# Kernel tuning notes

Hardware: AMD Instinct MI355X
Metric: run time of the kernel (lower is better)

## Reference

```python
import jax, jax.numpy as jnp
import numpy as np

T, B, E, H = 2048, 2, 2048, 16
HD = E // H
SCALE = HD ** -0.5
NEG = -1e9  # large-negative additive mask (finite, safe in fp32/bf16)


def setup_inputs() -> dict:
    key = jax.random.key(0)
    ks = jax.random.split(key, 6)
    query = jax.random.normal(ks[0], (T, B, E), dtype=jnp.float32)
    # causal additive mask, as metaseq builds for decoder self-attention
    attn_mask = jnp.where(jnp.tril(jnp.ones((T, T), dtype=bool)), 0.0, NEG).astype(jnp.float32)
    # combined qkv projection: rows ordered [K | V | Q] per split_tensor_along_last_dim
    qkv_w = jax.random.normal(ks[1], (3 * E, E), dtype=jnp.float32) * (1.0 / np.sqrt(2 * E))
    qkv_b = jax.random.uniform(ks[2], (3 * E,), dtype=jnp.float32, minval=-1, maxval=1) / np.sqrt(E)
    out_w = jax.random.normal(ks[3], (E, E), dtype=jnp.float32) * (1.0 / np.sqrt(2 * E))
    out_b = jax.random.uniform(ks[4], (E,), dtype=jnp.float32, minval=-1, maxval=1) / np.sqrt(E)
    return {"query": query, "attn_mask": attn_mask, "qkv_w": qkv_w,
            "qkv_b": qkv_b, "out_w": out_w, "out_b": out_b}


def reference(query, attn_mask, qkv_w, qkv_b, out_w, out_b):
    t, b, e = query.shape
    # fused QKV projection (ColumnParallelLinear, world_size=1)
    kvq = jnp.einsum('tbe,fe->tbf', query, qkv_w) + qkv_b  # [T,B,3E]
    k, v, q = kvq[..., :e], kvq[..., e:2 * e], kvq[..., 2 * e:]
    q = q * SCALE
    q = q.reshape(t, b, H, HD)
    k = k.reshape(t, b, H, HD)
    v = v.reshape(t, b, H, HD)
    # explicit QK^T bmm -> [B,H,T,S]
    scores = jnp.einsum('tbhd,sbhd->bhts', q, k) + attn_mask[None, None]
    probs = jax.nn.softmax(scores, axis=-1)  # dropout p=0 -> identity
    ctx = jnp.einsum('bhts,sbhd->tbhd', probs, v).reshape(t, b, e)
    # RowParallelLinear out_proj (skip_bias_add in the original; bias added here)
    out = jnp.einsum('tbe,fe->tbf', ctx, out_w) + out_b
    return out
```

## Files before the change

kernel.cpp:

```cpp
#include <hip/hip_runtime.h>
#include <hip/hip_bf16.h>
#include <stdint.h>

#define T_DIM 2048
#define B_DIM 2
#define E_DIM 2048
#define H_DIM 16
#define HD_DIM 128
#define F_DIM 6144
#define ROWS 4096
#define KVB 64

#define QK_SCALE 0.08838834764831845f
#define LOG2E    1.4426950408889634f
#define RESCALE_THR 8.0f

typedef __bf16 bf16_t;
typedef __bf16 bf16x8 __attribute__((ext_vector_type(8)));
typedef __bf16 bf16x4 __attribute__((ext_vector_type(4)));
typedef float  f32x4  __attribute__((ext_vector_type(4)));

__device__ __forceinline__ void gll16(const void* g, void* l) {
  __builtin_amdgcn_global_load_lds((const __attribute__((address_space(1))) void*)g,
                                   (__attribute__((address_space(3))) void*)l, 16, 0, 0);
}

__global__ void cvt_f32_bf16(const float* __restrict__ src, bf16_t* __restrict__ dst, int n4) {
  int i = blockIdx.x * blockDim.x + threadIdx.x;
  int stride = gridDim.x * blockDim.x;
  for (; i < n4; i += stride) {
    float4 v = ((const float4*)src)[i];
    bf16x4 o;
    o[0] = (bf16_t)v.x; o[1] = (bf16_t)v.y; o[2] = (bf16_t)v.z; o[3] = (bf16_t)v.w;
    ((bf16x4*)dst)[i] = o;
  }
}

template<int EPI>
__launch_bounds__(256, 2)
__global__ void gemm_bt(const bf16_t* __restrict__ A, const bf16_t* __restrict__ Bm,
                        const float* __restrict__ bias, void* __restrict__ Cout,
                        int N, int K, int nbn, float qscale, int qcol0)
{
  __shared__ __align__(16) bf16_t As[128][64];
  __shared__ __align__(16) bf16_t Bs[128][64];

  int bid = blockIdx.x;
  int nwg = gridDim.x;
  int cpx = nwg >> 3;
  int swz = (bid & 7) * cpx + (bid >> 3);
  int bm = swz / nbn, bn = swz % nbn;

  int tid = threadIdx.x;
  int lane = tid & 63, wid = tid >> 6;
  int lr = lane & 15, lg = lane >> 4;
  int wm = wid >> 1, wn = wid & 1;

  f32x4 acc[4][4] = {};

  int srow8 = tid >> 3;
  int schunk = tid & 7;

  const bf16_t* gA = A + (size_t)(bm * 128) * K;
  const bf16_t* gB = Bm + (size_t)(bn * 128) * K;

  for (int k0 = 0; k0 < K; k0 += 64) {
    #pragma unroll
    for (int i = 0; i < 4; ++i) {
      int row = i * 32 + srow8;
      int sc = schunk ^ (row & 7);
      gll16(gA + (size_t)row * K + k0 + sc * 8, &As[row][schunk * 8]);
    }
    #pragma unroll
    for (int i = 0; i < 4; ++i) {
      int row = i * 32 + srow8;
      int sc = schunk ^ (row & 7);
      gll16(gB + (size_t)row * K + k0 + sc * 8, &Bs[row][schunk * 8]);
    }
    __syncthreads();

    #pragma unroll
    for (int kk = 0; kk < 2; ++kk) {
      bf16x8 af[4], bfr[4];
      #pragma unroll
      for (int mi = 0; mi < 4; ++mi) {
        int row = wm * 64 + mi * 16 + lr;
        int ch = (kk * 4 + lg) ^ (row & 7);
        af[mi] = *(const bf16x8*)&As[row][ch * 8];
      }
      #pragma unroll
      for (int ni = 0; ni < 4; ++ni) {
        int row = wn * 64 + ni * 16 + lr;
        int ch = (kk * 4 + lg) ^ (row & 7);
        bfr[ni] = *(const bf16x8*)&Bs[row][ch * 8];
      }
      #pragma unroll
      for (int mi = 0; mi < 4; ++mi)
        #pragma unroll
        for (int ni = 0; ni < 4; ++ni)
          acc[mi][ni] = __builtin_amdgcn_mfma_f32_16x16x32_bf16(af[mi], bfr[ni], acc[mi][ni], 0, 0, 0);
    }
    __syncthreads();
  }

  #pragma unroll
  for (int mi = 0; mi < 4; ++mi) {
    int row0 = bm * 128 + wm * 64 + mi * 16 + lg * 4;
    #pragma unroll
    for (int ni = 0; ni < 4; ++ni) {
      int col = bn * 128 + wn * 64 + ni * 16 + lr;
      float bv = bias[col];
      float scl = (EPI == 0 && col >= qcol0) ? qscale : 1.0f;
      #pragma unroll
      for (int r = 0; r < 4; ++r) {
        float v = (acc[mi][ni][r] + bv) * scl;
        if (EPI == 0) ((bf16_t*)Cout)[(size_t)(row0 + r) * N + col] = (bf16_t)v;
        else          ((float*)Cout)[(size_t)(row0 + r) * N + col] = v;
      }
    }
  }
}

__global__ void repack_vt(const bf16_t* __restrict__ KVQ, bf16_t* __restrict__ VTg)
{
  __shared__ __align__(16) bf16_t tile[64][136];
  int bid = blockIdx.x;
  int st = bid & 31, bh = bid >> 5;
  int b = bh >> 4, h = bh & 15;
  int s0 = st * 64;
  int tid = threadIdx.x;

  const bf16_t* vbase = KVQ + (size_t)b * F_DIM + E_DIM + (size_t)h * HD_DIM;
  #pragma unroll
  for (int i = 0; i < 4; ++i) {
    int row = i * 16 + (tid >> 4), c = tid & 15;
    bf16x8 v = *(const bf16x8*)(vbase + (size_t)(s0 + row) * B_DIM * F_DIM + c * 8);
    *(bf16x8*)&tile[row][c * 8] = v;
  }
  __syncthreads();
  bf16_t* out = VTg + (size_t)bh * HD_DIM * T_DIM;
  #pragma unroll
  for (int i = 0; i < 4; ++i) {
    int d = i * 32 + (tid >> 3), c = tid & 7;
    bf16x8 o;
    #pragma unroll
    for (int j = 0; j < 8; ++j) o[j] = tile[c * 8 + j][d];
    *(bf16x8*)(out + (size_t)d * T_DIM + s0 + c * 8) = o;
  }
}

__launch_bounds__(256, 2)
__global__ void attn2(const bf16_t* __restrict__ KVQ, const bf16_t* __restrict__ VTg,
                      bf16_t* __restrict__ CTX)
{
  __shared__ __align__(16) bf16_t Ks[2][KVB][128];
  __shared__ __align__(16) bf16_t Vs[2][128][KVB];
  __shared__ __align__(16) bf16_t Ps[4][16][72];

  int bid = blockIdx.x;
  int cpx = gridDim.x >> 3;
  int swz = (bid & 7) * cpx + (bid >> 3);
  int qt = 31 - (swz & 31);
  int bh = swz >> 5;
  int b = bh >> 4, h = bh & 15;

  int tid = threadIdx.x;
  int lane = tid & 63, wid = tid >> 6;
  int lr = lane & 15, lg = lane >> 4;

  const bf16_t* kbase = KVQ + (size_t)b * F_DIM + (size_t)h * HD_DIM;
  const bf16_t* vtb   = VTg + (size_t)bh * HD_DIM * T_DIM;

  bf16x8 qf[4];
  {
    int t = qt * 64 + wid * 16 + lr;
    const bf16_t* qb = KVQ + ((size_t)t * B_DIM + b) * F_DIM + 2 * E_DIM + h * HD_DIM;
    #pragma unroll
    for (int ks = 0; ks < 4; ++ks) qf[ks] = *(const bf16x8*)(qb + ks * 32 + lg * 8);
  }

  f32x4 ctxa[8] = {};
  float m[4], lsum[4];
  #pragma unroll
  for (int r = 0; r < 4; ++r) { m[r] = -1e30f; lsum[r] = 0.0f; }

  int krow = tid >> 4, kch = tid & 15;
  int vrow = tid >> 3, vch = tid & 7;

  auto stage = [&](int buf, int it) {
    int s0 = it * KVB;
    #pragma unroll
    for (int i = 0; i < 4; ++i) {
      int row = i * 16 + krow;
      int sc = kch ^ (row & 7);
      gll16(kbase + (size_t)(s0 + row) * B_DIM * F_DIM + sc * 8, &Ks[buf][row][kch * 8]);
    }
    #pragma unroll
    for (int i = 0; i < 4; ++i) {
      int row = i * 32 + vrow;
      int sc = vch ^ (row & 7);
      gll16(vtb + (size_t)row * T_DIM + s0 + sc * 8, &Vs[buf][row][vch * 8]);
    }
  };

  int nt = qt + 1;
  stage(0, 0);
  __syncthreads();

  int tq = qt * 64 + wid * 16 + lg * 4;

  for (int it = 0; it < nt; ++it) {
    int cur = it & 1;
    if (it + 1 < nt) stage(cur ^ 1, it + 1);
    int s0 = it * KVB;
    bool diag = (it == nt - 1);

    f32x4 sacc[4] = {};
    __builtin_amdgcn_s_setprio(1);
    #pragma unroll
    for (int ks = 0; ks < 4; ++ks) {
      #pragma unroll
      for (int nti = 0; nti < 4; ++nti) {
        int srow = nti * 16 + lr;
        int slot = (ks * 4 + lg) ^ (srow & 7);
        bf16x8 kf = *(const bf16x8*)&Ks[cur][srow][slot * 8];
        sacc[nti] = __builtin_amdgcn_mfma_f32_16x16x32_bf16(qf[ks], kf, sacc[nti], 0, 0, 0);
      }
    }
    __builtin_amdgcn_s_setprio(0);

    float sv[4][4];
    float mxl = -1e30f;
    #pragma unroll
    for (int r = 0; r < 4; ++r) {
      #pragma unroll
      for (int nti = 0; nti < 4; ++nti) {
        float v = sacc[nti][r];
        if (diag) v = (s0 + nti * 16 + lr > tq + r) ? -1e30f : v;
        sv[r][nti] = v;
        mxl = fmaxf(mxl, v - m[r]);
      }
    }
    if (!__all(mxl <= RESCALE_THR)) {
      #pragma unroll
      for (int r = 0; r < 4; ++r) {
        float mx = fmaxf(fmaxf(sv[r][0], sv[r][1]), fmaxf(sv[r][2], sv[r][3]));
        #pragma unroll
        for (int d = 1; d < 16; d <<= 1) mx = fmaxf(mx, __shfl_xor(mx, d, 64));
        float mn = fmaxf(m[r], mx);
        float rs = exp2f(m[r] - mn);
        m[r] = mn;
        lsum[r] *= rs;
        #pragma unroll
        for (int dt = 0; dt < 8; ++dt) ctxa[dt][r] *= rs;
      }
    }
    #pragma unroll
    for (int r = 0; r < 4; ++r) {
      #pragma unroll
      for (int nti = 0; nti < 4; ++nti) {
        float p = exp2f(sv[r][nti] - m[r]);
        lsum[r] += p;
        Ps[wid][lg * 4 + r][nti * 16 + lr] = (bf16_t)p;
      }
    }
    asm volatile("s_waitcnt lgkmcnt(0)" ::: "memory");
    __builtin_amdgcn_sched_barrier(0);

    bf16x8 pf0 = *(const bf16x8*)&Ps[wid][lr][lg * 8];
    bf16x8 pf1 = *(const bf16x8*)&Ps[wid][lr][32 + lg * 8];
    __builtin_amdgcn_s_setprio(1);
    #pragma unroll
    for (int dt = 0; dt < 8; ++dt) {
      int drow = dt * 16 + lr;
      int sl0 = lg ^ (drow & 7);
      int sl1 = (4 + lg) ^ (drow & 7);
      bf16x8 vf0 = *(const bf16x8*)&Vs[cur][drow][sl0 * 8];
      bf16x8 vf1 = *(const bf16x8*)&Vs[cur][drow][sl1 * 8];
      ctxa[dt] = __builtin_amdgcn_mfma_f32_16x16x32_bf16(pf0, vf0, ctxa[dt], 0, 0, 0);
      ctxa[dt] = __builtin_amdgcn_mfma_f32_16x16x32_bf16(pf1, vf1, ctxa[dt], 0, 0, 0);
    }
    __builtin_amdgcn_s_setprio(0);

    __syncthreads();
  }

  #pragma unroll
  for (int r = 0; r < 4; ++r) {
    #pragma unroll
    for (int d = 1; d < 16; d <<= 1) lsum[r] += __shfl_xor(lsum[r], d, 64);
  }

  #pragma unroll
  for (int r = 0; r < 4; ++r) {
    int t = qt * 64 + wid * 16 + lg * 4 + r;
    float inv = 1.0f / lsum[r];
    bf16_t* out = CTX + ((size_t)t * B_DIM + b) * E_DIM + h * HD_DIM;
    #pragma unroll
    for (int dt = 0; dt < 8; ++dt)
      out[dt * 16 + lr] = (bf16_t)(ctxa[dt][r] * inv);
  }
}

extern "C" void kernel_launch(void* const* d_in, const int* in_sizes, int n_in,
                              void* d_out, int out_size, void* d_ws, size_t ws_size,
                              hipStream_t stream)
{
  const float* query = (const float*)d_in[0];
  const float* qkv_w = (const float*)d_in[2];
  const float* qkv_b = (const float*)d_in[3];
  const float* out_w = (const float*)d_in[4];
  const float* out_b = (const float*)d_in[5];

  bf16_t* Xbf  = (bf16_t*)d_ws;
  bf16_t* Wqkv = Xbf  + (size_t)ROWS * E_DIM;
  bf16_t* Wout = Wqkv + (size_t)F_DIM * E_DIM;
  bf16_t* KVQ  = Wout + (size_t)E_DIM * E_DIM;
  bf16_t* CTX  = Xbf;
  bf16_t* VTg  = Wqkv;

  cvt_f32_bf16<<<2048, 256, 0, stream>>>(query, Xbf,  ROWS * E_DIM / 4);
  cvt_f32_bf16<<<2048, 256, 0, stream>>>(qkv_w, Wqkv, F_DIM * E_DIM / 4);
  cvt_f32_bf16<<<2048, 256, 0, stream>>>(out_w, Wout, E_DIM * E_DIM / 4);

  gemm_bt<0><<<32 * 48, 256, 0, stream>>>(Xbf, Wqkv, qkv_b, KVQ,
                                          F_DIM, E_DIM, 48, QK_SCALE * LOG2E, 2 * E_DIM);

  repack_vt<<<32 * 32, 256, 0, stream>>>(KVQ, VTg);

  attn2<<<B_DIM * H_DIM * (T_DIM / 64), 256, 0, stream>>>(KVQ, VTg, CTX);

  gemm_bt<1><<<32 * 16, 256, 0, stream>>>(CTX, Wout, out_b, (float*)d_out,
                                          E_DIM, E_DIM, 16, 1.0f, 1 << 30);
}
```

Before: 303.5 us.

## Double attention query tile to 128 rows per block with new XCD-aware scheduling

The attention kernel now handles 128 query rows per block (32 per wave, two MFMA row fragments), so each staged K/V tile feeds twice as many MFMAs. This halves the global K/V traffic per query and the number of blocks to 512. Blocks are remapped so each XCD owns four (batch, head) pairs, with heavy and light causal tiles paired within a slot. The P scratch buffer gets an XOR-swizzled layout. In exchange, per-wave register pressure roughly doubles for accumulators, and fewer blocks may reduce occupancy and worsen tail balance.

```diff
diff --git a/kernel.cpp b/kernel.cpp
--- a/kernel.cpp
+++ b/kernel.cpp
@@ -150,18 +150,21 @@
 }
 
 __launch_bounds__(256, 2)
-__global__ void attn2(const bf16_t* __restrict__ KVQ, const bf16_t* __restrict__ VTg,
+__global__ void attn3(const bf16_t* __restrict__ KVQ, const bf16_t* __restrict__ VTg,
                       bf16_t* __restrict__ CTX)
 {
   __shared__ __align__(16) bf16_t Ks[2][KVB][128];
   __shared__ __align__(16) bf16_t Vs[2][128][KVB];
-  __shared__ __align__(16) bf16_t Ps[4][16][72];
+  __shared__ __align__(16) bf16_t Ps[4][32 * 64];
 
   int bid = blockIdx.x;
-  int cpx = gridDim.x >> 3;
-  int swz = (bid & 7) * cpx + (bid >> 3);
-  int qt = 31 - (swz & 31);
-  int bh = swz >> 5;
+  int xcd = bid & 7;
+  int j   = bid >> 3;
+  int hi  = j >> 5;
+  int mid = (j >> 4) & 1;
+  int q   = j & 15;
+  int bh  = xcd * 4 + hi * 2 + mid;
+  int qt  = hi ? (15 - q) : q;
   int b = bh >> 4, h = bh & 15;
 
   int tid = threadIdx.x;
@@ -170,19 +173,23 @@
 
   const bf16_t* kbase = KVQ + (size_t)b * F_DIM + (size_t)h * HD_DIM;
   const bf16_t* vtb   = VTg + (size_t)bh * HD_DIM * T_DIM;
-
-  bf16x8 qf[4];
-  {
-    int t = qt * 64 + wid * 16 + lr;
+  bf16_t* PsW = &Ps[wid][0];
+
+  bf16x8 qf[2][4];
+  #pragma unroll
+  for (int mf = 0; mf < 2; ++mf) {
+    int t = qt * 128 + wid * 32 + mf * 16 + lr;
     const bf16_t* qb = KVQ + ((size_t)t * B_DIM + b) * F_DIM + 2 * E_DIM + h * HD_DIM;
     #pragma unroll
-    for (int ks = 0; ks < 4; ++ks) qf[ks] = *(const bf16x8*)(qb + ks * 32 + lg * 8);
-  }
-
-  f32x4 ctxa[8] = {};
-  float m[4], lsum[4];
-  #pragma unroll
-  for (int r = 0; r < 4; ++r) { m[r] = -1e30f; lsum[r] = 0.0f; }
+    for (int ks = 0; ks < 4; ++ks) qf[mf][ks] = *(const bf16x8*)(qb + ks * 32 + lg * 8);
+  }
+
+  f32x4 ctxa[2][8] = {};
+  float m[2][4], lsum[2][4];
+  #pragma unroll
+  for (int mf = 0; mf < 2; ++mf)
+    #pragma unroll
+    for (int r = 0; r < 4; ++r) { m[mf][r] = -1e30f; lsum[mf][r] = 0.0f; }
 
   int krow = tid >> 4, kch = tid & 15;
   int vrow = tid >> 3, vch = tid & 7;
@@ -203,19 +210,19 @@
     }
   };
 
-  int nt = qt + 1;
+  int nt = 2 * (qt + 1);
   stage(0, 0);
   __syncthreads();
 
-  int tq = qt * 64 + wid * 16 + lg * 4;
+  int tqw = qt * 128 + wid * 32;
 
   for (int it = 0; it < nt; ++it) {
     int cur = it & 1;
     if (it + 1 < nt) stage(cur ^ 1, it + 1);
     int s0 = it * KVB;
-    bool diag = (it == nt - 1);
-
-    f32x4 sacc[4] = {};
+    bool diag = (it >= nt - 2);
+
+    f32x4 sacc[2][4] = {};
     __builtin_amdgcn_s_setprio(1);
     #pragma unroll
     for (int ks = 0; ks < 4; ++ks) {
@@ -224,51 +231,67 @@
         int srow = nti * 16 + lr;
         int slot = (ks * 4 + lg) ^ (srow & 7);
         bf16x8 kf = *(const bf16x8*)&Ks[cur][srow][slot * 8];
-        sacc[nti] = __builtin_amdgcn_mfma_f32_16x16x32_bf16(qf[ks], kf, sacc[nti], 0, 0, 0);
+        sacc[0][nti] = __builtin_amdgcn_mfma_f32_16x16x32_bf16(qf[0][ks], kf, sacc[0][nti], 0, 0, 0);
+        sacc[1][nti] = __builtin_amdgcn_mfma_f32_16x16x32_bf16(qf[1][ks], kf, sacc[1][nti], 0, 0, 0);
       }
     }
     __builtin_amdgcn_s_setprio(0);
 
-    float sv[4][4];
     float mxl = -1e30f;
     #pragma unroll
-    for (int r = 0; r < 4; ++r) {
-      #pragma unroll
-      for (int nti = 0; nti < 4; ++nti) {
-        float v = sacc[nti][r];
-        if (diag) v = (s0 + nti * 16 + lr > tq + r) ? -1e30f : v;
-        sv[r][nti] = v;
-        mxl = fmaxf(mxl, v - m[r]);
-      }
-    }
+    for (int mf = 0; mf < 2; ++mf)
+      #pragma unroll
+      for (int r = 0; r < 4; ++r)
+        #pragma unroll
+        for (int nti = 0; nti < 4; ++nti) {
+          float v = sacc[mf][nti][r];
+          if (diag) v = (s0 + nti * 16 + lr > tqw + mf * 16 + lg * 4 + r) ? -1e30f : v;
+          sacc[mf][nti][r] = v;
+          mxl = fmaxf(mxl, v - m[mf][r]);
+        }
     if (!__all(mxl <= RESCALE_THR)) {
       #pragma unroll
+      for (int mf = 0; mf < 2; ++mf)
+        #pragma unroll
+        for (int r = 0; r < 4; ++r) {
+          float mx = fmaxf(fmaxf(sacc[mf][0][r], sacc[mf][1][r]),
+                           fmaxf(sacc[mf][2][r], sacc[mf][3][r]));
+          #pragma unroll
+          for (int d = 1; d < 16; d <<= 1) mx = fmaxf(mx, __shfl_xor(mx, d, 64));
+          float mn = fmaxf(m[mf][r], mx);
+          float rs = exp2f(m[mf][r] - mn);
+          m[mf][r] = mn;
+          lsum[mf][r] *= rs;
+          #pragma unroll
+          for (int dt = 0; dt < 8; ++dt) ctxa[mf][dt][r] *= rs;
+        }
+    }
+    #pragma unroll
+    for (int mf = 0; mf < 2; ++mf)
+      #pragma unroll
       for (int r = 0; r < 4; ++r) {
-        float mx = fmaxf(fmaxf(sv[r][0], sv[r][1]), fmaxf(sv[r][2], sv[r][3]));
+        int prow = mf * 16 + lg * 4 + r;
         #pragma unroll
-        for (int d = 1; d < 16; d <<= 1) mx = fmaxf(mx, __shfl_xor(mx, d, 64));
-        float mn = fmaxf(m[r], mx);
-        float rs = exp2f(m[r] - mn);
-        m[r] = mn;
-        lsum[r] *= rs;
-        #pragma unroll
-        for (int dt = 0; dt < 8; ++dt) ctxa[dt][r] *= rs;
-      }
-    }
-    #pragma unroll
-    for (int r = 0; r < 4; ++r) {
-      #pragma unroll
-      for (int nti = 0; nti < 4; ++nti) {
-        float p = exp2f(sv[r][nti] - m[r]);
-        lsum[r] += p;
-        Ps[wid][lg * 4 + r][nti * 16 + lr] = (bf16_t)p;
-      }
-    }
+        for (int nti = 0; nti < 4; ++nti) {
+          float p = exp2f(sacc[mf][nti][r] - m[mf][r]);
+          lsum[mf][r] += p;
+          int chk = (nti * 2 + (lr >> 3)) ^ (prow & 7);
+          PsW[prow * 64 + chk * 8 + (lr & 7)] = (bf16_t)p;
+        }
+      }
     asm volatile("s_waitcnt lgkmcnt(0)" ::: "memory");
     __builtin_amdgcn_sched_barrier(0);
 
-    bf16x8 pf0 = *(const bf16x8*)&Ps[wid][lr][lg * 8];
-    bf16x8 pf1 = *(const bf16x8*)&Ps[wid][lr][32 + lg * 8];
+    bf16x8 pf[2][2];
+    #pragma unroll
+    for (int mf = 0; mf < 2; ++mf) {
+      int prow = mf * 16 + lr;
+      #pragma unroll
+      for (int kh = 0; kh < 2; ++kh) {
+        int chk = (kh * 4 + lg) ^ (prow & 7);
+        pf[mf][kh] = *(const bf16x8*)&PsW[prow * 64 + chk * 8];
+      }
+    }
     __builtin_amdgcn_s_setprio(1);
     #pragma unroll
     for (int dt = 0; dt < 8; ++dt) {
@@ -277,8 +300,10 @@
       int sl1 = (4 + lg) ^ (drow & 7);
       bf16x8 vf0 = *(const bf16x8*)&Vs[cur][drow][sl0 * 8];
       bf16x8 vf1 = *(const bf16x8*)&Vs[cur][drow][sl1 * 8];
-      ctxa[dt] = __builtin_amdgcn_mfma_f32_16x16x32_bf16(pf0, vf0, ctxa[dt], 0, 0, 0);
-      ctxa[dt] = __builtin_amdgcn_mfma_f32_16x16x32_bf16(pf1, vf1, ctxa[dt], 0, 0, 0);
+      ctxa[0][dt] = __builtin_amdgcn_mfma_f32_16x16x32_bf16(pf[0][0], vf0, ctxa[0][dt], 0, 0, 0);
+      ctxa[0][dt] = __builtin_amdgcn_mfma_f32_16x16x32_bf16(pf[0][1], vf1, ctxa[0][dt], 0, 0, 0);
+      ctxa[1][dt] = __builtin_amdgcn_mfma_f32_16x16x32_bf16(pf[1][0], vf0, ctxa[1][dt], 0, 0, 0);
+      ctxa[1][dt] = __builtin_amdgcn_mfma_f32_16x16x32_bf16(pf[1][1], vf1, ctxa[1][dt], 0, 0, 0);
     }
     __builtin_amdgcn_s_setprio(0);
 
@@ -286,20 +311,24 @@
   }
 
   #pragma unroll
-  for (int r = 0; r < 4; ++r) {
-    #pragma unroll
-    for (int d = 1; d < 16; d <<= 1) lsum[r] += __shfl_xor(lsum[r], d, 64);
-  }
-
-  #pragma unroll
-  for (int r = 0; r < 4; ++r) {
-    int t = qt * 64 + wid * 16 + lg * 4 + r;
-    float inv = 1.0f / lsum[r];
-    bf16_t* out = CTX + ((size_t)t * B_DIM + b) * E_DIM + h * HD_DIM;
-    #pragma unroll
-    for (int dt = 0; dt < 8; ++dt)
-      out[dt * 16 + lr] = (bf16_t)(ctxa[dt][r] * inv);
-  }
+  for (int mf = 0; mf < 2; ++mf)
+    #pragma unroll
+    for (int r = 0; r < 4; ++r) {
+      #pragma unroll
+      for (int d = 1; d < 16; d <<= 1) lsum[mf][r] += __shfl_xor(lsum[mf][r], d, 64);
+    }
+
+  #pragma unroll
+  for (int mf = 0; mf < 2; ++mf)
+    #pragma unroll
+    for (int r = 0; r < 4; ++r) {
+      int t = qt * 128 + wid * 32 + mf * 16 + lg * 4 + r;
+      float inv = 1.0f / lsum[mf][r];
+      bf16_t* out = CTX + ((size_t)t * B_DIM + b) * E_DIM + h * HD_DIM;
+      #pragma unroll
+      for (int dt = 0; dt < 8; ++dt)
+        out[dt * 16 + lr] = (bf16_t)(ctxa[mf][dt][r] * inv);
+    }
 }
 
 extern "C" void kernel_launch(void* const* d_in, const int* in_sizes, int n_in,
@@ -328,7 +357,7 @@
 
   repack_vt<<<32 * 32, 256, 0, stream>>>(KVQ, VTg);
 
-  attn2<<<B_DIM * H_DIM * (T_DIM / 64), 256, 0, stream>>>(KVQ, VTg, CTX);
+  attn3<<<512, 256, 0, stream>>>(KVQ, VTg, CTX);
 
   gemm_bt<1><<<32 * 16, 256, 0, stream>>>(CTX, Wout, out_b, (float*)d_out,
                                           E_DIM, E_DIM, 16, 1.0f, 1 << 30);
```

Result: faster. 281.7 us (-7.2%).
